# Optimization experiments

Measured on AMD Instinct MI355X. Metric: run time of the kernel, lower is better.

The kernel has to match this reference:

```python
import jax, jax.numpy as jnp
import numpy as np

B, T, D, H = 8, 1024, 768, 12
HD = D // H  # head_dim = 64


def setup_inputs() -> dict:
    key = jax.random.key(0)
    ks = jax.random.split(key, 6)
    s = 1.0 / np.sqrt(D)
    return {
        "x": jax.random.normal(ks[0], (B, T, D), dtype=jnp.float32),
        "Wq": jax.random.normal(ks[1], (D, D), dtype=jnp.float32) * s,
        "Wk": jax.random.normal(ks[2], (D, D), dtype=jnp.float32) * s,
        "Wv": jax.random.normal(ks[3], (D, D), dtype=jnp.float32) * s,
        "Wp": jax.random.normal(ks[4], (D, D), dtype=jnp.float32) * s,
        "bp": jnp.zeros((D,), dtype=jnp.float32),
    }


def reference(x, Wq, Wk, Wv, Wp, bp):
    Bx, Tx, Dx = x.shape
    # projections (nn.Linear applies x @ W.T; weights here are stored as [out,in]-equivalent square)
    q = (x @ Wq.T).reshape(Bx, Tx, H, HD).transpose(0, 2, 1, 3)  # [B,H,T,hd]
    k = (x @ Wk.T).reshape(Bx, Tx, H, HD).transpose(0, 2, 1, 3)
    v = (x @ Wv.T).reshape(Bx, Tx, H, HD).transpose(0, 2, 1, 3)
    scores = jnp.einsum("bhqd,bhkd->bhqk", q, k)  # raw QK^T, then mask, then scale (as in source)
    causal = jnp.tril(jnp.ones((Tx, Tx), dtype=bool))
    scores = jnp.where(causal, scores, -jnp.inf)
    weights = jax.nn.softmax(scores / np.sqrt(HD), axis=-1)
    # dropout is identity in eval mode
    ctx = jnp.einsum("bhqk,bhkd->bhqd", weights, v)
    ctx = ctx.transpose(0, 2, 1, 3).reshape(Bx, Tx, Dx)
    return ctx @ Wp.T + bp
```

## Files before the change

kernel.cpp:

```cpp
#include <hip/hip_runtime.h>
#include <hip/hip_bf16.h>
#include <math.h>

#define Bsz 8
#define Tsz 1024
#define Dsz 768
#define Hn  12
#define Msz (Bsz*Tsz)
#define NQT (Tsz/64)

typedef __attribute__((ext_vector_type(8))) short bf16x8_t;
typedef __attribute__((ext_vector_type(4))) float f32x4_t;

__device__ __forceinline__ unsigned short f2bf(float f) {
  unsigned u = __builtin_bit_cast(unsigned, f);
  u += 0x7FFFu + ((u >> 16) & 1u);
  return (unsigned short)(u >> 16);
}

__device__ __forceinline__ unsigned short f2bf_fast(float f) {
  __hip_bfloat16 h = __float2bfloat16(f);
  return __builtin_bit_cast(unsigned short, h);
}

__device__ __forceinline__ void gload16(const void* g, const void* l) {
  __builtin_amdgcn_global_load_lds(
      (const __attribute__((address_space(1))) unsigned int*)g,
      (__attribute__((address_space(3))) unsigned int*)l, 16, 0, 0);
}

#define XBLKS (Msz*Dsz/1024)
#define WBLKS (Dsz*Dsz/1024)
__global__ __launch_bounds__(256) void cvt_all_kernel(
    const float* __restrict__ x,
    const float* __restrict__ w0, const float* __restrict__ w1,
    const float* __restrict__ w2, const float* __restrict__ w3,
    unsigned short* __restrict__ xb,
    unsigned short* __restrict__ o0, unsigned short* __restrict__ o1,
    unsigned short* __restrict__ o2, unsigned short* __restrict__ o3) {
  int bid = blockIdx.x;
  const float* src; unsigned short* dst; size_t blk;
  if (bid < XBLKS) { src = x; dst = xb; blk = bid; }
  else {
    int t = bid - XBLKS;
    int which = t / WBLKS;
    blk = t % WBLKS;
    switch (which) {
      case 0: src = w0; dst = o0; break;
      case 1: src = w1; dst = o1; break;
      case 2: src = w2; dst = o2; break;
      default: src = w3; dst = o3; break;
    }
  }
  size_t idx = (blk * 256 + threadIdx.x) * 4;
  float4 v = *(const float4*)(src + idx);
  union { unsigned short u[4]; uint2 w; } t;
  t.u[0] = f2bf(v.x); t.u[1] = f2bf(v.y); t.u[2] = f2bf(v.z); t.u[3] = f2bf(v.w);
  *(uint2*)(dst + idx) = t.w;
}

__global__ __launch_bounds__(256) void gemm_qkv_kernel(
    const unsigned short* __restrict__ X, const unsigned short* __restrict__ Wcat,
    unsigned short* __restrict__ Yq, unsigned short* __restrict__ Yk,
    unsigned short* __restrict__ Yvt) {
  __shared__ __align__(16) unsigned short As[128 * 32];
  __shared__ __align__(16) unsigned short Bs[128 * 32];
  const int tid = threadIdx.x;
  const int w = tid >> 6, lane = tid & 63;
  const int i = lane & 15, g = lane >> 4;
  const int wr = w >> 1, wc = w & 1;
  const int bm = blockIdx.x * 128, bn = blockIdx.y * 128;

  f32x4_t acc[4][4];
  #pragma unroll
  for (int a = 0; a < 4; ++a)
    #pragma unroll
    for (int b2 = 0; b2 < 4; ++b2)
      #pragma unroll
      for (int r = 0; r < 4; ++r) acc[a][b2][r] = 0.f;

  for (int k0 = 0; k0 < Dsz; k0 += 32) {
    __syncthreads();
    #pragma unroll
    for (int j = 0; j < 2; ++j) {
      const int c = 2 * w + j;
      const int row = 16 * c + (lane >> 2);
      const int cb = (lane & 3) * 16;
      gload16((const char*)X + ((size_t)(bm + row) * Dsz + k0) * 2 + cb,
              (const char*)As + c * 1024);
      gload16((const char*)Wcat + ((size_t)(bn + row) * Dsz + k0) * 2 + cb,
              (const char*)Bs + c * 1024);
    }
    __syncthreads();
    bf16x8_t af[4], bfr[4];
    #pragma unroll
    for (int f = 0; f < 4; ++f) {
      af[f]  = *(const bf16x8_t*)&As[(64 * wr + 16 * f + i) * 32 + 8 * g];
      bfr[f] = *(const bf16x8_t*)&Bs[(64 * wc + 16 * f + i) * 32 + 8 * g];
    }
    #pragma unroll
    for (int a = 0; a < 4; ++a)
      #pragma unroll
      for (int b2 = 0; b2 < 4; ++b2)
        acc[a][b2] = __builtin_amdgcn_mfma_f32_16x16x32_bf16(af[a], bfr[b2], acc[a][b2], 0, 0, 0);
  }

  const int wsel = blockIdx.y / 6;
  const int nloc = (blockIdx.y % 6) * 128;
  if (wsel < 2) {
    unsigned short* Y = wsel ? Yk : Yq;
    const float sc = wsel ? 1.0f : 0.18033688f;
    #pragma unroll
    for (int fi = 0; fi < 4; ++fi)
      #pragma unroll
      for (int fj = 0; fj < 4; ++fj) {
        const int n = nloc + 64 * wc + 16 * fj + i;
        #pragma unroll
        for (int r = 0; r < 4; ++r) {
          const int m = bm + 64 * wr + 16 * fi + 4 * g + r;
          Y[(size_t)m * Dsz + n] = f2bf_fast(acc[fi][fj][r] * sc);
        }
      }
  } else {
    #pragma unroll
    for (int fi = 0; fi < 4; ++fi)
      #pragma unroll
      for (int fj = 0; fj < 4; ++fj) {
        const int m0 = bm + 64 * wr + 16 * fi + 4 * g;
        const int bb = m0 >> 10;
        const int t  = m0 & 1023;
        const int n  = nloc + 64 * wc + 16 * fj + i;
        union { unsigned short u[4]; uint2 v; } pk;
        #pragma unroll
        for (int r = 0; r < 4; ++r) pk.u[r] = f2bf_fast(acc[fi][fj][r]);
        *(uint2*)&Yvt[((size_t)(bb * Dsz + n)) * Tsz + t] = pk.v;
      }
  }
}

__global__ __launch_bounds__(256) void gemm_proj_kernel(
    const unsigned short* __restrict__ X, const unsigned short* __restrict__ W,
    const float* __restrict__ bias, float* __restrict__ Y) {
  __shared__ __align__(16) unsigned short As[128 * 32];
  __shared__ __align__(16) unsigned short Bs[128 * 32];
  const int tid = threadIdx.x;
  const int w = tid >> 6, lane = tid & 63;
  const int i = lane & 15, g = lane >> 4;
  const int wr = w >> 1, wc = w & 1;
  const int bm = blockIdx.x * 128, bn = blockIdx.y * 128;

  f32x4_t acc[4][4];
  #pragma unroll
  for (int a = 0; a < 4; ++a)
    #pragma unroll
    for (int b2 = 0; b2 < 4; ++b2)
      #pragma unroll
      for (int r = 0; r < 4; ++r) acc[a][b2][r] = 0.f;

  for (int k0 = 0; k0 < Dsz; k0 += 32) {
    __syncthreads();
    #pragma unroll
    for (int j = 0; j < 2; ++j) {
      const int c = 2 * w + j;
      const int row = 16 * c + (lane >> 2);
      const int cb = (lane & 3) * 16;
      gload16((const char*)X + ((size_t)(bm + row) * Dsz + k0) * 2 + cb,
              (const char*)As + c * 1024);
      gload16((const char*)W + ((size_t)(bn + row) * Dsz + k0) * 2 + cb,
              (const char*)Bs + c * 1024);
    }
    __syncthreads();
    bf16x8_t af[4], bfr[4];
    #pragma unroll
    for (int f = 0; f < 4; ++f) {
      af[f]  = *(const bf16x8_t*)&As[(64 * wr + 16 * f + i) * 32 + 8 * g];
      bfr[f] = *(const bf16x8_t*)&Bs[(64 * wc + 16 * f + i) * 32 + 8 * g];
    }
    #pragma unroll
    for (int a = 0; a < 4; ++a)
      #pragma unroll
      for (int b2 = 0; b2 < 4; ++b2)
        acc[a][b2] = __builtin_amdgcn_mfma_f32_16x16x32_bf16(af[a], bfr[b2], acc[a][b2], 0, 0, 0);
  }

  #pragma unroll
  for (int fi = 0; fi < 4; ++fi)
    #pragma unroll
    for (int fj = 0; fj < 4; ++fj) {
      const int n = bn + 64 * wc + 16 * fj + i;
      const float bv = bias[n];
      #pragma unroll
      for (int r = 0; r < 4; ++r) {
        const int m = bm + 64 * wr + 16 * fi + 4 * g + r;
        Y[(size_t)m * Dsz + n] = acc[fi][fj][r] + bv;
      }
    }
}

__global__ __launch_bounds__(256) void attn_mfma_kernel(
    const unsigned short* __restrict__ Qm, const unsigned short* __restrict__ Km,
    const unsigned short* __restrict__ Vt, unsigned short* __restrict__ ctx) {
  __shared__ __align__(16) unsigned short Ks[2][64 * 64];
  __shared__ __align__(16) unsigned short Vs[2][64 * 64];
  __shared__ __align__(16) unsigned short Ps[4][16 * 72];
  const int tid = threadIdx.x, w = tid >> 6, lane = tid & 63;
  const int i = lane & 15, g = lane >> 4;
  const int bh = blockIdx.y, b = bh / Hn, h = bh % Hn;
  const int qtA = blockIdx.x, qtB = NQT - 1 - qtA;
  const int ntot = qtA + qtB + 2;

  const int sr  = lane >> 3;
  const int swz = ((lane & 7) * 16) ^ (sr << 4);

  bf16x8_t qa[2][2];
  #pragma unroll
  for (int ts = 0; ts < 2; ++ts) {
    const int t0 = (ts ? qtB : qtA) * 64;
    const unsigned short* qp =
        Qm + ((size_t)(b * Tsz + t0 + 16 * w + i) * Dsz + h * 64 + 8 * g);
    qa[ts][0] = *(const bf16x8_t*)qp;
    qa[ts][1] = *(const bf16x8_t*)(qp + 32);
  }

  f32x4_t o[4];
  #pragma unroll
  for (int fd = 0; fd < 4; ++fd)
    #pragma unroll
    for (int r = 0; r < 4; ++r) o[fd][r] = 0.f;
  float mrun[4] = {-3.0e38f, -3.0e38f, -3.0e38f, -3.0e38f};
  float lrun[4] = {0.f, 0.f, 0.f, 0.f};

  auto STAGE = [&](int kv0, int p) {
    #pragma unroll
    for (int j = 0; j < 2; ++j) {
      const int c = 2 * w + j;
      const int row = 8 * c + sr;
      gload16((const char*)Km + ((size_t)(b * Tsz + kv0 + row) * Dsz + h * 64) * 2 + swz,
              (const char*)Ks[p] + c * 1024);
      gload16((const char*)Vt + ((size_t)(bh * 64 + row) * Tsz + kv0) * 2 + swz,
              (const char*)Vs[p] + c * 1024);
    }
  };

  STAGE(0, 0);

  unsigned short* Pw = &Ps[w][0];

  for (int fi = 0; fi < ntot; ++fi) {
    const int p = fi & 1;
    const int ts = (fi > qtA) ? 1 : 0;
    const int qt = ts ? qtB : qtA;
    const int t0 = qt * 64;
    const int kt = ts ? (fi - qtA - 1) : fi;

    __syncthreads();

    if (fi + 1 < ntot) {
      const int nf = fi + 1;
      const int nkt = (nf > qtA) ? (nf - qtA - 1) : nf;
      STAGE(nkt * 64, p ^ 1);
    }

    f32x4_t s[4];
    __builtin_amdgcn_s_setprio(1);
    #pragma unroll
    for (int fj = 0; fj < 4; ++fj) {
      #pragma unroll
      for (int r = 0; r < 4; ++r) s[fj][r] = 0.f;
      const int R = 16 * fj + i;
      #pragma unroll
      for (int ks = 0; ks < 2; ++ks) {
        const bf16x8_t kb = *(const bf16x8_t*)((const char*)Ks[p] + R * 128 +
                                               ((64 * ks + 16 * g) ^ ((i & 7) << 4)));
        s[fj] = __builtin_amdgcn_mfma_f32_16x16x32_bf16(qa[ts][ks], kb, s[fj], 0, 0, 0);
      }
    }
    __builtin_amdgcn_s_setprio(0);

    if (kt == qt) {
      #pragma unroll
      for (int fj = 0; fj < 4; ++fj) {
        const int kidx = kt * 64 + 16 * fj + i;
        #pragma unroll
        for (int r = 0; r < 4; ++r)
          if (kidx > t0 + 16 * w + 4 * g + r) s[fj][r] = -1.0e30f;
      }
    }

    float mx[4];
    #pragma unroll
    for (int r = 0; r < 4; ++r)
      mx[r] = fmaxf(fmaxf(s[0][r], s[1][r]), fmaxf(s[2][r], s[3][r]));
    #pragma unroll
    for (int r = 0; r < 4; ++r) {
      mx[r] = fmaxf(mx[r], __shfl_xor(mx[r], 1));
      mx[r] = fmaxf(mx[r], __shfl_xor(mx[r], 2));
      mx[r] = fmaxf(mx[r], __shfl_xor(mx[r], 4));
      mx[r] = fmaxf(mx[r], __shfl_xor(mx[r], 8));
    }

    bool nd = false;
    #pragma unroll
    for (int r = 0; r < 4; ++r) nd = nd || (mx[r] > mrun[r] + 8.0f);
    if (__any(nd)) {
      #pragma unroll
      for (int r = 0; r < 4; ++r) {
        const float mn = fmaxf(mrun[r], mx[r]);
        const float fs = exp2f(mrun[r] - mn);
        mrun[r] = mn;
        lrun[r] *= fs;
        #pragma unroll
        for (int fd = 0; fd < 4; ++fd) o[fd][r] *= fs;
      }
    }

    float rs[4] = {0.f, 0.f, 0.f, 0.f};
    #pragma unroll
    for (int fj = 0; fj < 4; ++fj)
      #pragma unroll
      for (int r = 0; r < 4; ++r) {
        s[fj][r] = exp2f(s[fj][r] - mrun[r]);
        rs[r] += s[fj][r];
      }
    #pragma unroll
    for (int r = 0; r < 4; ++r) {
      rs[r] += __shfl_xor(rs[r], 1);
      rs[r] += __shfl_xor(rs[r], 2);
      rs[r] += __shfl_xor(rs[r], 4);
      rs[r] += __shfl_xor(rs[r], 8);
      lrun[r] += rs[r];
    }

    #pragma unroll
    for (int fj = 0; fj < 4; ++fj)
      #pragma unroll
      for (int r = 0; r < 4; ++r)
        Pw[(4 * g + r) * 72 + 16 * fj + i] = f2bf_fast(s[fj][r]);

    __builtin_amdgcn_s_setprio(1);
    #pragma unroll
    for (int ks = 0; ks < 2; ++ks) {
      const bf16x8_t pa = *(const bf16x8_t*)&Pw[i * 72 + 32 * ks + 8 * g];
      #pragma unroll
      for (int fd = 0; fd < 4; ++fd) {
        const int R = 16 * fd + i;
        const bf16x8_t vb = *(const bf16x8_t*)((const char*)Vs[p] + R * 128 +
                                               ((64 * ks + 16 * g) ^ ((i & 7) << 4)));
        o[fd] = __builtin_amdgcn_mfma_f32_16x16x32_bf16(pa, vb, o[fd], 0, 0, 0);
      }
    }
    __builtin_amdgcn_s_setprio(0);

    if (fi == qtA) {
      #pragma unroll
      for (int r = 0; r < 4; ++r) {
        const float inv = 1.f / lrun[r];
        const int qidx = t0 + 16 * w + 4 * g + r;
        #pragma unroll
        for (int fd = 0; fd < 4; ++fd)
          ctx[(size_t)(b * Tsz + qidx) * Dsz + h * 64 + 16 * fd + i] =
              f2bf_fast(o[fd][r] * inv);
      }
      #pragma unroll
      for (int fd = 0; fd < 4; ++fd)
        #pragma unroll
        for (int r = 0; r < 4; ++r) o[fd][r] = 0.f;
      #pragma unroll
      for (int r = 0; r < 4; ++r) { mrun[r] = -3.0e38f; lrun[r] = 0.f; }
    }
  }

  {
    const int t0 = qtB * 64;
    #pragma unroll
    for (int r = 0; r < 4; ++r) {
      const float inv = 1.f / lrun[r];
      const int qidx = t0 + 16 * w + 4 * g + r;
      #pragma unroll
      for (int fd = 0; fd < 4; ++fd)
        ctx[(size_t)(b * Tsz + qidx) * Dsz + h * 64 + 16 * fd + i] =
            f2bf_fast(o[fd][r] * inv);
    }
  }
}

extern "C" void kernel_launch(void* const* d_in, const int* in_sizes, int n_in,
                              void* d_out, int out_size, void* d_ws, size_t ws_size,
                              hipStream_t stream) {
  const float* x  = (const float*)d_in[0];
  const float* Wq = (const float*)d_in[1];
  const float* Wk = (const float*)d_in[2];
  const float* Wv = (const float*)d_in[3];
  const float* Wp = (const float*)d_in[4];
  const float* bp = (const float*)d_in[5];
  float* out = (float*)d_out;

  const size_t md = (size_t)Msz * Dsz;
  const size_t wd = (size_t)Dsz * Dsz;
  unsigned short* xb   = (unsigned short*)d_ws;
  unsigned short* wqb  = xb + md;
  unsigned short* wkb  = wqb + wd;
  unsigned short* wvb  = wkb + wd;
  unsigned short* wpb  = wvb + wd;
  unsigned short* qb   = wpb + wd;
  unsigned short* kb   = qb + md;
  unsigned short* vtb  = kb + md;
  unsigned short* ctxb = vtb + md;

  cvt_all_kernel<<<XBLKS + 4 * WBLKS, 256, 0, stream>>>(
      x, Wq, Wk, Wv, Wp, xb, wqb, wkb, wvb, wpb);

  gemm_qkv_kernel<<<dim3(Msz / 128, 18), 256, 0, stream>>>(xb, wqb, qb, kb, vtb);

  attn_mfma_kernel<<<dim3(NQT / 2, Bsz * Hn), 256, 0, stream>>>(qb, kb, vtb, ctxb);

  gemm_proj_kernel<<<dim3(Msz / 128, Dsz / 128), 256, 0, stream>>>(ctxb, wpb, bp, out);
}
```

Before: 206.5 us.

## Widen GEMM K-tile with swizzled LDS and restructure attention into 8-wave adjacent-tile blocks

Both GEMM kernels now stage a 64-wide K slice per iteration into XOR-swizzled shared memory. This halves the number of barrier pairs and is meant to cut LDS bank conflicts on fragment reads. The attention kernel changes from pairing a short and a long query tile in one 4-wave block to 512-thread blocks, where two 4-wave groups handle adjacent query tiles and share each staged K/V tile. The grid is reordered so blocks of the same batch-head are launched together. This brings back causal load imbalance across blocks and leaves the lower group idle on the last KV tile, in exchange for sharing K/V loads and giving more waves per block.

```diff
diff --git a/kernel.cpp b/kernel.cpp
--- a/kernel.cpp
+++ b/kernel.cpp
@@ -63,13 +63,15 @@
     const unsigned short* __restrict__ X, const unsigned short* __restrict__ Wcat,
     unsigned short* __restrict__ Yq, unsigned short* __restrict__ Yk,
     unsigned short* __restrict__ Yvt) {
-  __shared__ __align__(16) unsigned short As[128 * 32];
-  __shared__ __align__(16) unsigned short Bs[128 * 32];
+  __shared__ __align__(16) unsigned short As[128 * 64];
+  __shared__ __align__(16) unsigned short Bs[128 * 64];
   const int tid = threadIdx.x;
   const int w = tid >> 6, lane = tid & 63;
   const int i = lane & 15, g = lane >> 4;
   const int wr = w >> 1, wc = w & 1;
   const int bm = blockIdx.x * 128, bn = blockIdx.y * 128;
+  const int sr = lane >> 3;
+  const int scb = ((lane & 7) * 16) ^ (sr << 4);
 
   f32x4_t acc[4][4];
   #pragma unroll
@@ -79,30 +81,40 @@
       #pragma unroll
       for (int r = 0; r < 4; ++r) acc[a][b2][r] = 0.f;
 
-  for (int k0 = 0; k0 < Dsz; k0 += 32) {
+  for (int k0 = 0; k0 < Dsz; k0 += 64) {
     __syncthreads();
     #pragma unroll
-    for (int j = 0; j < 2; ++j) {
-      const int c = 2 * w + j;
-      const int row = 16 * c + (lane >> 2);
-      const int cb = (lane & 3) * 16;
-      gload16((const char*)X + ((size_t)(bm + row) * Dsz + k0) * 2 + cb,
+    for (int j = 0; j < 4; ++j) {
+      const int c = 4 * w + j;
+      const int row = 8 * c + sr;
+      gload16((const char*)X + ((size_t)(bm + row) * Dsz + k0) * 2 + scb,
               (const char*)As + c * 1024);
-      gload16((const char*)Wcat + ((size_t)(bn + row) * Dsz + k0) * 2 + cb,
+      gload16((const char*)Wcat + ((size_t)(bn + row) * Dsz + k0) * 2 + scb,
               (const char*)Bs + c * 1024);
     }
     __syncthreads();
-    bf16x8_t af[4], bfr[4];
+    bf16x8_t af[4][2];
     #pragma unroll
     for (int f = 0; f < 4; ++f) {
-      af[f]  = *(const bf16x8_t*)&As[(64 * wr + 16 * f + i) * 32 + 8 * g];
-      bfr[f] = *(const bf16x8_t*)&Bs[(64 * wc + 16 * f + i) * 32 + 8 * g];
-    }
-    #pragma unroll
-    for (int a = 0; a < 4; ++a)
-      #pragma unroll
-      for (int b2 = 0; b2 < 4; ++b2)
-        acc[a][b2] = __builtin_amdgcn_mfma_f32_16x16x32_bf16(af[a], bfr[b2], acc[a][b2], 0, 0, 0);
+      const int R = 64 * wr + 16 * f + i;
+      #pragma unroll
+      for (int kk = 0; kk < 2; ++kk)
+        af[f][kk] = *(const bf16x8_t*)((const char*)As + R * 128 +
+                                       ((64 * kk + 16 * g) ^ ((i & 7) << 4)));
+    }
+    #pragma unroll
+    for (int b2 = 0; b2 < 4; ++b2) {
+      const int R = 64 * wc + 16 * b2 + i;
+      const bf16x8_t b0 = *(const bf16x8_t*)((const char*)Bs + R * 128 +
+                                             ((16 * g) ^ ((i & 7) << 4)));
+      const bf16x8_t b1 = *(const bf16x8_t*)((const char*)Bs + R * 128 +
+                                             ((64 + 16 * g) ^ ((i & 7) << 4)));
+      #pragma unroll
+      for (int a = 0; a < 4; ++a) {
+        acc[a][b2] = __builtin_amdgcn_mfma_f32_16x16x32_bf16(af[a][0], b0, acc[a][b2], 0, 0, 0);
+        acc[a][b2] = __builtin_amdgcn_mfma_f32_16x16x32_bf16(af[a][1], b1, acc[a][b2], 0, 0, 0);
+      }
+    }
   }
 
   const int wsel = blockIdx.y / 6;
@@ -141,13 +153,15 @@
 __global__ __launch_bounds__(256) void gemm_proj_kernel(
     const unsigned short* __restrict__ X, const unsigned short* __restrict__ W,
     const float* __restrict__ bias, float* __restrict__ Y) {
-  __shared__ __align__(16) unsigned short As[128 * 32];
-  __shared__ __align__(16) unsigned short Bs[128 * 32];
+  __shared__ __align__(16) unsigned short As[128 * 64];
+  __shared__ __align__(16) unsigned short Bs[128 * 64];
   const int tid = threadIdx.x;
   const int w = tid >> 6, lane = tid & 63;
   const int i = lane & 15, g = lane >> 4;
   const int wr = w >> 1, wc = w & 1;
   const int bm = blockIdx.x * 128, bn = blockIdx.y * 128;
+  const int sr = lane >> 3;
+  const int scb = ((lane & 7) * 16) ^ (sr << 4);
 
   f32x4_t acc[4][4];
   #pragma unroll
@@ -157,30 +171,40 @@
       #pragma unroll
       for (int r = 0; r < 4; ++r) acc[a][b2][r] = 0.f;
 
-  for (int k0 = 0; k0 < Dsz; k0 += 32) {
+  for (int k0 = 0; k0 < Dsz; k0 += 64) {
     __syncthreads();
     #pragma unroll
-    for (int j = 0; j < 2; ++j) {
-      const int c = 2 * w + j;
-      const int row = 16 * c + (lane >> 2);
-      const int cb = (lane & 3) * 16;
-      gload16((const char*)X + ((size_t)(bm + row) * Dsz + k0) * 2 + cb,
+    for (int j = 0; j < 4; ++j) {
+      const int c = 4 * w + j;
+      const int row = 8 * c + sr;
+      gload16((const char*)X + ((size_t)(bm + row) * Dsz + k0) * 2 + scb,
               (const char*)As + c * 1024);
-      gload16((const char*)W + ((size_t)(bn + row) * Dsz + k0) * 2 + cb,
+      gload16((const char*)W + ((size_t)(bn + row) * Dsz + k0) * 2 + scb,
               (const char*)Bs + c * 1024);
     }
     __syncthreads();
-    bf16x8_t af[4], bfr[4];
+    bf16x8_t af[4][2];
     #pragma unroll
     for (int f = 0; f < 4; ++f) {
-      af[f]  = *(const bf16x8_t*)&As[(64 * wr + 16 * f + i) * 32 + 8 * g];
-      bfr[f] = *(const bf16x8_t*)&Bs[(64 * wc + 16 * f + i) * 32 + 8 * g];
-    }
-    #pragma unroll
-    for (int a = 0; a < 4; ++a)
-      #pragma unroll
-      for (int b2 = 0; b2 < 4; ++b2)
-        acc[a][b2] = __builtin_amdgcn_mfma_f32_16x16x32_bf16(af[a], bfr[b2], acc[a][b2], 0, 0, 0);
+      const int R = 64 * wr + 16 * f + i;
+      #pragma unroll
+      for (int kk = 0; kk < 2; ++kk)
+        af[f][kk] = *(const bf16x8_t*)((const char*)As + R * 128 +
+                                       ((64 * kk + 16 * g) ^ ((i & 7) << 4)));
+    }
+    #pragma unroll
+    for (int b2 = 0; b2 < 4; ++b2) {
+      const int R = 64 * wc + 16 * b2 + i;
+      const bf16x8_t b0 = *(const bf16x8_t*)((const char*)Bs + R * 128 +
+                                             ((16 * g) ^ ((i & 7) << 4)));
+      const bf16x8_t b1 = *(const bf16x8_t*)((const char*)Bs + R * 128 +
+                                             ((64 + 16 * g) ^ ((i & 7) << 4)));
+      #pragma unroll
+      for (int a = 0; a < 4; ++a) {
+        acc[a][b2] = __builtin_amdgcn_mfma_f32_16x16x32_bf16(af[a][0], b0, acc[a][b2], 0, 0, 0);
+        acc[a][b2] = __builtin_amdgcn_mfma_f32_16x16x32_bf16(af[a][1], b1, acc[a][b2], 0, 0, 0);
+      }
+    }
   }
 
   #pragma unroll
@@ -197,29 +221,30 @@
     }
 }
 
-__global__ __launch_bounds__(256) void attn_mfma_kernel(
+__global__ __launch_bounds__(512) void attn_mfma_kernel(
     const unsigned short* __restrict__ Qm, const unsigned short* __restrict__ Km,
     const unsigned short* __restrict__ Vt, unsigned short* __restrict__ ctx) {
   __shared__ __align__(16) unsigned short Ks[2][64 * 64];
   __shared__ __align__(16) unsigned short Vs[2][64 * 64];
-  __shared__ __align__(16) unsigned short Ps[4][16 * 72];
+  __shared__ __align__(16) unsigned short Ps[8][16 * 72];
   const int tid = threadIdx.x, w = tid >> 6, lane = tid & 63;
   const int i = lane & 15, g = lane >> 4;
-  const int bh = blockIdx.y, b = bh / Hn, h = bh % Hn;
-  const int qtA = blockIdx.x, qtB = NQT - 1 - qtA;
-  const int ntot = qtA + qtB + 2;
+  const int grp = w >> 2, wl = w & 3;
+  const int bh = blockIdx.x, b = bh / Hn, h = bh % Hn;
+  const int j = blockIdx.y;
+  const int qt = 2 * j + grp;
+  const int t0 = qt * 64;
+  const int ntB = 2 * j + 2;
 
   const int sr  = lane >> 3;
   const int swz = ((lane & 7) * 16) ^ (sr << 4);
 
-  bf16x8_t qa[2][2];
-  #pragma unroll
-  for (int ts = 0; ts < 2; ++ts) {
-    const int t0 = (ts ? qtB : qtA) * 64;
+  bf16x8_t qa[2];
+  {
     const unsigned short* qp =
-        Qm + ((size_t)(b * Tsz + t0 + 16 * w + i) * Dsz + h * 64 + 8 * g);
-    qa[ts][0] = *(const bf16x8_t*)qp;
-    qa[ts][1] = *(const bf16x8_t*)(qp + 32);
+        Qm + ((size_t)(b * Tsz + t0 + 16 * wl + i) * Dsz + h * 64 + 8 * g);
+    qa[0] = *(const bf16x8_t*)qp;
+    qa[1] = *(const bf16x8_t*)(qp + 32);
   }
 
   f32x4_t o[4];
@@ -231,156 +256,122 @@
   float lrun[4] = {0.f, 0.f, 0.f, 0.f};
 
   auto STAGE = [&](int kv0, int p) {
-    #pragma unroll
-    for (int j = 0; j < 2; ++j) {
-      const int c = 2 * w + j;
-      const int row = 8 * c + sr;
-      gload16((const char*)Km + ((size_t)(b * Tsz + kv0 + row) * Dsz + h * 64) * 2 + swz,
-              (const char*)Ks[p] + c * 1024);
-      gload16((const char*)Vt + ((size_t)(bh * 64 + row) * Tsz + kv0) * 2 + swz,
-              (const char*)Vs[p] + c * 1024);
-    }
+    const int row = 8 * w + sr;
+    gload16((const char*)Km + ((size_t)(b * Tsz + kv0 + row) * Dsz + h * 64) * 2 + swz,
+            (const char*)Ks[p] + w * 1024);
+    gload16((const char*)Vt + ((size_t)(bh * 64 + row) * Tsz + kv0) * 2 + swz,
+            (const char*)Vs[p] + w * 1024);
   };
 
   STAGE(0, 0);
-
   unsigned short* Pw = &Ps[w][0];
 
-  for (int fi = 0; fi < ntot; ++fi) {
-    const int p = fi & 1;
-    const int ts = (fi > qtA) ? 1 : 0;
-    const int qt = ts ? qtB : qtA;
-    const int t0 = qt * 64;
-    const int kt = ts ? (fi - qtA - 1) : fi;
-
+  for (int kt = 0; kt < ntB; ++kt) {
+    const int p = kt & 1;
     __syncthreads();
-
-    if (fi + 1 < ntot) {
-      const int nf = fi + 1;
-      const int nkt = (nf > qtA) ? (nf - qtA - 1) : nf;
-      STAGE(nkt * 64, p ^ 1);
-    }
-
-    f32x4_t s[4];
-    __builtin_amdgcn_s_setprio(1);
-    #pragma unroll
-    for (int fj = 0; fj < 4; ++fj) {
-      #pragma unroll
-      for (int r = 0; r < 4; ++r) s[fj][r] = 0.f;
-      const int R = 16 * fj + i;
+    if (kt + 1 < ntB) STAGE((kt + 1) * 64, p ^ 1);
+
+    if (kt <= qt) {
+      f32x4_t s[4];
+      __builtin_amdgcn_s_setprio(1);
+      #pragma unroll
+      for (int fj = 0; fj < 4; ++fj) {
+        #pragma unroll
+        for (int r = 0; r < 4; ++r) s[fj][r] = 0.f;
+        const int R = 16 * fj + i;
+        #pragma unroll
+        for (int ks = 0; ks < 2; ++ks) {
+          const bf16x8_t kb = *(const bf16x8_t*)((const char*)Ks[p] + R * 128 +
+                                                 ((64 * ks + 16 * g) ^ ((i & 7) << 4)));
+          s[fj] = __builtin_amdgcn_mfma_f32_16x16x32_bf16(qa[ks], kb, s[fj], 0, 0, 0);
+        }
+      }
+      __builtin_amdgcn_s_setprio(0);
+
+      if (kt == qt) {
+        #pragma unroll
+        for (int fj = 0; fj < 4; ++fj) {
+          const int kidx = kt * 64 + 16 * fj + i;
+          #pragma unroll
+          for (int r = 0; r < 4; ++r)
+            if (kidx > t0 + 16 * wl + 4 * g + r) s[fj][r] = -1.0e30f;
+        }
+      }
+
+      float mx[4];
+      #pragma unroll
+      for (int r = 0; r < 4; ++r)
+        mx[r] = fmaxf(fmaxf(s[0][r], s[1][r]), fmaxf(s[2][r], s[3][r]));
+      #pragma unroll
+      for (int r = 0; r < 4; ++r) {
+        mx[r] = fmaxf(mx[r], __shfl_xor(mx[r], 1));
+        mx[r] = fmaxf(mx[r], __shfl_xor(mx[r], 2));
+        mx[r] = fmaxf(mx[r], __shfl_xor(mx[r], 4));
+        mx[r] = fmaxf(mx[r], __shfl_xor(mx[r], 8));
+      }
+
+      bool nd = false;
+      #pragma unroll
+      for (int r = 0; r < 4; ++r) nd = nd || (mx[r] > mrun[r] + 8.0f);
+      if (__any(nd)) {
+        #pragma unroll
+        for (int r = 0; r < 4; ++r) {
+          const float mn = fmaxf(mrun[r], mx[r]);
+          const float fs = exp2f(mrun[r] - mn);
+          mrun[r] = mn;
+          lrun[r] *= fs;
+          #pragma unroll
+          for (int fd = 0; fd < 4; ++fd) o[fd][r] *= fs;
+        }
+      }
+
+      float rs[4] = {0.f, 0.f, 0.f, 0.f};
+      #pragma unroll
+      for (int fj = 0; fj < 4; ++fj)
+        #pragma unroll
+        for (int r = 0; r < 4; ++r) {
+          s[fj][r] = exp2f(s[fj][r] - mrun[r]);
+          rs[r] += s[fj][r];
+        }
+      #pragma unroll
+      for (int r = 0; r < 4; ++r) {
+        rs[r] += __shfl_xor(rs[r], 1);
+        rs[r] += __shfl_xor(rs[r], 2);
+        rs[r] += __shfl_xor(rs[r], 4);
+        rs[r] += __shfl_xor(rs[r], 8);
+        lrun[r] += rs[r];
+      }
+
+      #pragma unroll
+      for (int fj = 0; fj < 4; ++fj)
+        #pragma unroll
+        for (int r = 0; r < 4; ++r)
+          Pw[(4 * g + r) * 72 + 16 * fj + i] = f2bf_fast(s[fj][r]);
+
+      __builtin_amdgcn_s_setprio(1);
       #pragma unroll
       for (int ks = 0; ks < 2; ++ks) {
-        const bf16x8_t kb = *(const bf16x8_t*)((const char*)Ks[p] + R * 128 +
-                                               ((64 * ks + 16 * g) ^ ((i & 7) << 4)));
-        s[fj] = __builtin_amdgcn_mfma_f32_16x16x32_bf16(qa[ts][ks], kb, s[fj], 0, 0, 0);
-      }
-    }
-    __builtin_amdgcn_s_setprio(0);
-
-    if (kt == qt) {
-      #pragma unroll
-      for (int fj = 0; fj < 4; ++fj) {
-        const int kidx = kt * 64 + 16 * fj + i;
-        #pragma unroll
-        for (int r = 0; r < 4; ++r)
-          if (kidx > t0 + 16 * w + 4 * g + r) s[fj][r] = -1.0e30f;
-      }
-    }
-
-    float mx[4];
-    #pragma unroll
-    for (int r = 0; r < 4; ++r)
-      mx[r] = fmaxf(fmaxf(s[0][r], s[1][r]), fmaxf(s[2][r], s[3][r]));
-    #pragma unroll
-    for (int r = 0; r < 4; ++r) {
-      mx[r] = fmaxf(mx[r], __shfl_xor(mx[r], 1));
-      mx[r] = fmaxf(mx[r], __shfl_xor(mx[r], 2));
-      mx[r] = fmaxf(mx[r], __shfl_xor(mx[r], 4));
-      mx[r] = fmaxf(mx[r], __shfl_xor(mx[r], 8));
-    }
-
-    bool nd = false;
-    #pragma unroll
-    for (int r = 0; r < 4; ++r) nd = nd || (mx[r] > mrun[r] + 8.0f);
-    if (__any(nd)) {
-      #pragma unroll
-      for (int r = 0; r < 4; ++r) {
-        const float mn = fmaxf(mrun[r], mx[r]);
-        const float fs = exp2f(mrun[r] - mn);
-        mrun[r] = mn;
-        lrun[r] *= fs;
-        #pragma unroll
-        for (int fd = 0; fd < 4; ++fd) o[fd][r] *= fs;
-      }
-    }
-
-    float rs[4] = {0.f, 0.f, 0.f, 0.f};
-    #pragma unroll
-    for (int fj = 0; fj < 4; ++fj)
-      #pragma unroll
-      for (int r = 0; r < 4; ++r) {
-        s[fj][r] = exp2f(s[fj][r] - mrun[r]);
-        rs[r] += s[fj][r];
-      }
-    #pragma unroll
-    for (int r = 0; r < 4; ++r) {
-      rs[r] += __shfl_xor(rs[r], 1);
-      rs[r] += __shfl_xor(rs[r], 2);
-      rs[r] += __shfl_xor(rs[r], 4);
-      rs[r] += __shfl_xor(rs[r], 8);
-      lrun[r] += rs[r];
-    }
-
-    #pragma unroll
-    for (int fj = 0; fj < 4; ++fj)
-      #pragma unroll
-      for (int r = 0; r < 4; ++r)
-        Pw[(4 * g + r) * 72 + 16 * fj + i] = f2bf_fast(s[fj][r]);
-
-    __builtin_amdgcn_s_setprio(1);
-    #pragma unroll
-    for (int ks = 0; ks < 2; ++ks) {
-      const bf16x8_t pa = *(const bf16x8_t*)&Pw[i * 72 + 32 * ks + 8 * g];
-      #pragma unroll
-      for (int fd = 0; fd < 4; ++fd) {
-        const int R = 16 * fd + i;
-        const bf16x8_t vb = *(const bf16x8_t*)((const char*)Vs[p] + R * 128 +
-                                               ((64 * ks + 16 * g) ^ ((i & 7) << 4)));
-        o[fd] = __builtin_amdgcn_mfma_f32_16x16x32_bf16(pa, vb, o[fd], 0, 0, 0);
-      }
-    }
-    __builtin_amdgcn_s_setprio(0);
-
-    if (fi == qtA) {
-      #pragma unroll
-      for (int r = 0; r < 4; ++r) {
-        const float inv = 1.f / lrun[r];
-        const int qidx = t0 + 16 * w + 4 * g + r;
-        #pragma unroll
-        for (int fd = 0; fd < 4; ++fd)
-          ctx[(size_t)(b * Tsz + qidx) * Dsz + h * 64 + 16 * fd + i] =
-              f2bf_fast(o[fd][r] * inv);
-      }
-      #pragma unroll
-      for (int fd = 0; fd < 4; ++fd)
-        #pragma unroll
-        for (int r = 0; r < 4; ++r) o[fd][r] = 0.f;
-      #pragma unroll
-      for (int r = 0; r < 4; ++r) { mrun[r] = -3.0e38f; lrun[r] = 0.f; }
-    }
-  }
-
-  {
-    const int t0 = qtB * 64;
-    #pragma unroll
-    for (int r = 0; r < 4; ++r) {
-      const float inv = 1.f / lrun[r];
-      const int qidx = t0 + 16 * w + 4 * g + r;
-      #pragma unroll
-      for (int fd = 0; fd < 4; ++fd)
-        ctx[(size_t)(b * Tsz + qidx) * Dsz + h * 64 + 16 * fd + i] =
-            f2bf_fast(o[fd][r] * inv);
-    }
+        const bf16x8_t pa = *(const bf16x8_t*)&Pw[i * 72 + 32 * ks + 8 * g];
+        #pragma unroll
+        for (int fd = 0; fd < 4; ++fd) {
+          const int R = 16 * fd + i;
+          const bf16x8_t vb = *(const bf16x8_t*)((const char*)Vs[p] + R * 128 +
+                                                 ((64 * ks + 16 * g) ^ ((i & 7) << 4)));
+          o[fd] = __builtin_amdgcn_mfma_f32_16x16x32_bf16(pa, vb, o[fd], 0, 0, 0);
+        }
+      }
+      __builtin_amdgcn_s_setprio(0);
+    }
+  }
+
+  #pragma unroll
+  for (int r = 0; r < 4; ++r) {
+    const float inv = 1.f / lrun[r];
+    const int qidx = t0 + 16 * wl + 4 * g + r;
+    #pragma unroll
+    for (int fd = 0; fd < 4; ++fd)
+      ctx[(size_t)(b * Tsz + qidx) * Dsz + h * 64 + 16 * fd + i] =
+          f2bf_fast(o[fd][r] * inv);
   }
 }
 
@@ -412,7 +403,7 @@
 
   gemm_qkv_kernel<<<dim3(Msz / 128, 18), 256, 0, stream>>>(xb, wqb, qb, kb, vtb);
 
-  attn_mfma_kernel<<<dim3(NQT / 2, Bsz * Hn), 256, 0, stream>>>(qb, kb, vtb, ctxb);
+  attn_mfma_kernel<<<dim3(Bsz * Hn, 8), 512, 0, stream>>>(qb, kb, vtb, ctxb);
 
   gemm_proj_kernel<<<dim3(Msz / 128, Dsz / 128), 256, 0, stream>>>(ctxb, wpb, bp, out);
 }
```

Result: slower. 211.4 us (+2.4%).
